# Optimization experiments

Hardware: AMD Instinct MI355X
Metric: run time of the kernel (lower is better)

## Reference

```python
import jax, jax.numpy as jnp
import numpy as np

EPS = 1e-8  # torch F.cosine_similarity default eps


def setup_inputs() -> dict:
    key = jax.random.key(0)
    k1, k2 = jax.random.split(key)
    xs_pad = jax.random.normal(k1, (8, 4096, 512), dtype=jnp.float32)
    spk_emb = jax.random.normal(k2, (8, 256, 512), dtype=jnp.float32)
    return {"xs_pad": xs_pad, "spk_emb": spk_emb}


def reference(xs_pad, spk_emb):
    # Faithful to F.cosine_similarity(x.unsqueeze(2), y.unsqueeze(1), dim=-1):
    #   dot(x, y) / (max(||x||, eps) * max(||y||, eps))
    # Implemented as L2-normalize then a batched GEMM -> (B, T, S), avoiding
    # the (B, T, S, D) broadcast intermediate.
    x_norm = jnp.maximum(jnp.linalg.norm(xs_pad, axis=-1, keepdims=True), EPS)
    y_norm = jnp.maximum(jnp.linalg.norm(spk_emb, axis=-1, keepdims=True), EPS)
    xn = xs_pad / x_norm          # (B, T, D)
    yn = spk_emb / y_norm         # (B, S, D)
    scores = jnp.einsum('btd,bsd->bts', xn, yn)  # (B, T, S)
    return scores
```

## Files before the change

### kernel.cpp

```cpp
#include <hip/hip_runtime.h>
#include <hip/hip_bf16.h>

#define BB 8
#define TT 4096
#define SS 256
#define DD 512
#define XROWS (BB * TT)
#define YROWS (BB * SS)

typedef __attribute__((ext_vector_type(8))) short short8;
typedef __attribute__((ext_vector_type(4))) float floatx4;

__device__ inline short f2bf(float f) {
  unsigned u = __builtin_bit_cast(unsigned, f);
  u += 0x7fffu + ((u >> 16) & 1u);
  return (short)(u >> 16);
}

__device__ inline short8 cvt8(float4 f0, float4 f1) {
  short8 o;
  o[0] = f2bf(f0.x);
  o[1] = f2bf(f0.y);
  o[2] = f2bf(f0.z);
  o[3] = f2bf(f0.w);
  o[4] = f2bf(f1.x);
  o[5] = f2bf(f1.y);
  o[6] = f2bf(f1.z);
  o[7] = f2bf(f1.w);
  return o;
}

__global__ __launch_bounds__(256) void cos_scale_kernel(
    const float* __restrict__ xs, const float* __restrict__ spk,
    float* __restrict__ xscale, float* __restrict__ yscale) {
  const int wave = threadIdx.x >> 6;
  const int lane = threadIdx.x & 63;
  int row = blockIdx.x * 4 + wave;
  const float* src;
  float* dst;
  if (row < XROWS) {
    src = xs + (size_t)row * DD;
    dst = xscale + row;
  } else {
    int r = row - XROWS;
    src = spk + (size_t)r * DD;
    dst = yscale + r;
  }
  const float4* s4 = (const float4*)src + lane * 2;
  float4 a = s4[0];
  float4 b = s4[1];
  float ss = a.x * a.x + a.y * a.y + a.z * a.z + a.w * a.w +
             b.x * b.x + b.y * b.y + b.z * b.z + b.w * b.w;
#pragma unroll
  for (int off = 32; off; off >>= 1) ss += __shfl_xor(ss, off, 64);
  if (lane == 0) *dst = 1.0f / fmaxf(sqrtf(ss), 1e-8f);
}

__global__ __launch_bounds__(256) void cos_gemm_kernel(
    const float* __restrict__ xs, const float* __restrict__ spk,
    const float* __restrict__ xscale, const float* __restrict__ yscale,
    float* __restrict__ out) {
  __shared__ float sA[128 * 64];
  __shared__ float sB[128 * 64];

  const int tid = threadIdx.x;
  const int wave = tid >> 6;
  const int lane = tid & 63;
  const int tn = blockIdx.x;
  const int tm = blockIdx.y;
  const int b = blockIdx.z;

  const float* Abase = xs + ((size_t)b * TT + tm * 128) * DD;
  const float* Bbase = spk + ((size_t)b * SS + tn * 128) * DD;

  floatx4 acc[4][4];
#pragma unroll
  for (int i = 0; i < 4; i++)
#pragma unroll
    for (int j = 0; j < 4; j++) acc[i][j] = (floatx4){0.f, 0.f, 0.f, 0.f};

  const int wm = wave >> 1;
  const int wn = wave & 1;
  const int quad = lane >> 4;
  const int l15 = lane & 15;

  int aoff[8];
#pragma unroll
  for (int j = 0; j < 8; j++) {
    int s = j * 256 + tid;
    int row = s >> 4;
    int blk = (s & 15) ^ (row & 15);
    aoff[j] = row * DD + blk * 4;
  }

  for (int kt = 0; kt < DD / 64; ++kt) {
#pragma unroll
    for (int j = 0; j < 8; j++) {
      const float* ga = Abase + aoff[j] + kt * 64;
      const float* gb = Bbase + aoff[j] + kt * 64;
      __builtin_amdgcn_global_load_lds(
          (const __attribute__((address_space(1))) unsigned int*)ga,
          (__attribute__((address_space(3))) unsigned int*)(sA +
              (j * 256 + wave * 64) * 4),
          16, 0, 0);
      __builtin_amdgcn_global_load_lds(
          (const __attribute__((address_space(1))) unsigned int*)gb,
          (__attribute__((address_space(3))) unsigned int*)(sB +
              (j * 256 + wave * 64) * 4),
          16, 0, 0);
    }
    __syncthreads();

#pragma unroll
    for (int ks = 0; ks < 2; ks++) {
      short8 af[4], bf[4];
      const int b0 = ks * 8 + quad * 2;
#pragma unroll
      for (int im = 0; im < 4; im++) {
        int row = wm * 64 + im * 16 + l15;
        int s0 = b0 ^ (row & 15);
        int s1 = (b0 + 1) ^ (row & 15);
        float4 f0 = *(const float4*)(sA + row * 64 + s0 * 4);
        float4 f1 = *(const float4*)(sA + row * 64 + s1 * 4);
        af[im] = cvt8(f0, f1);
      }
#pragma unroll
      for (int in = 0; in < 4; in++) {
        int row = wn * 64 + in * 16 + l15;
        int s0 = b0 ^ (row & 15);
        int s1 = (b0 + 1) ^ (row & 15);
        float4 f0 = *(const float4*)(sB + row * 64 + s0 * 4);
        float4 f1 = *(const float4*)(sB + row * 64 + s1 * 4);
        bf[in] = cvt8(f0, f1);
      }
#pragma unroll
      for (int im = 0; im < 4; im++)
#pragma unroll
        for (int in = 0; in < 4; in++)
          acc[im][in] = __builtin_amdgcn_mfma_f32_16x16x32_bf16(
              af[im], bf[in], acc[im][in], 0, 0, 0);
    }
    __syncthreads();
  }

  float* Obase = out + ((size_t)b * TT + tm * 128) * SS + tn * 128;
  const float* xsc = xscale + b * TT + tm * 128;
  const float* ysc = yscale + b * SS + tn * 128;
#pragma unroll
  for (int im = 0; im < 4; im++) {
#pragma unroll
    for (int in = 0; in < 4; in++) {
      int col = wn * 64 + in * 16 + l15;
      float yv = ysc[col];
#pragma unroll
      for (int r = 0; r < 4; r++) {
        int row = wm * 64 + im * 16 + quad * 4 + r;
        Obase[row * SS + col] = acc[im][in][r] * xsc[row] * yv;
      }
    }
  }
}

extern "C" void kernel_launch(void* const* d_in, const int* in_sizes, int n_in,
                              void* d_out, int out_size, void* d_ws,
                              size_t ws_size, hipStream_t stream) {
  const float* xs = (const float*)d_in[0];
  const float* spk = (const float*)d_in[1];
  float* out = (float*)d_out;

  float* xscale = (float*)d_ws;
  float* yscale = xscale + XROWS;

  hipLaunchKernelGGL(cos_scale_kernel, dim3((XROWS + YROWS) / 4), dim3(256), 0,
                     stream, xs, spk, xscale, yscale);
  hipLaunchKernelGGL(cos_gemm_kernel, dim3(SS / 128, TT / 128, BB), dim3(256),
                     0, stream, xs, spk, xscale, yscale, out);
}
```

Measured before the change: 124.9 us.

## Fuse row-norm computation into GEMM kernel using LDS-resident tiles

Removes the separate norm-scale kernel and computes the squared row norms of both operands inside the GEMM from the fp32 tiles already loaded into shared memory. Partial sums are reduced across lane quads with shuffles and stored as reciprocal scales in shared memory for the epilogue. This eliminates a full extra pass over the large input, a workspace round trip and one kernel launch. In exchange it adds extra FMA work per tile, more registers, and a redundant computation of the same norms by each tile sharing a row.

After: 123.8 us. About the same (-0.9%).

```diff
diff --git a/kernel.cpp b/kernel.cpp
--- a/kernel.cpp
+++ b/kernel.cpp
@@ -5,8 +5,6 @@
 #define TT 4096
 #define SS 256
 #define DD 512
-#define XROWS (BB * TT)
-#define YROWS (BB * SS)
 
 typedef __attribute__((ext_vector_type(8))) short short8;
 typedef __attribute__((ext_vector_type(4))) float floatx4;
@@ -30,38 +28,18 @@
   return o;
 }
 
-__global__ __launch_bounds__(256) void cos_scale_kernel(
-    const float* __restrict__ xs, const float* __restrict__ spk,
-    float* __restrict__ xscale, float* __restrict__ yscale) {
-  const int wave = threadIdx.x >> 6;
-  const int lane = threadIdx.x & 63;
-  int row = blockIdx.x * 4 + wave;
-  const float* src;
-  float* dst;
-  if (row < XROWS) {
-    src = xs + (size_t)row * DD;
-    dst = xscale + row;
-  } else {
-    int r = row - XROWS;
-    src = spk + (size_t)r * DD;
-    dst = yscale + r;
-  }
-  const float4* s4 = (const float4*)src + lane * 2;
-  float4 a = s4[0];
-  float4 b = s4[1];
-  float ss = a.x * a.x + a.y * a.y + a.z * a.z + a.w * a.w +
-             b.x * b.x + b.y * b.y + b.z * b.z + b.w * b.w;
-#pragma unroll
-  for (int off = 32; off; off >>= 1) ss += __shfl_xor(ss, off, 64);
-  if (lane == 0) *dst = 1.0f / fmaxf(sqrtf(ss), 1e-8f);
+__device__ inline float sq8(float4 f0, float4 f1) {
+  return f0.x * f0.x + f0.y * f0.y + f0.z * f0.z + f0.w * f0.w +
+         f1.x * f1.x + f1.y * f1.y + f1.z * f1.z + f1.w * f1.w;
 }
 
-__global__ __launch_bounds__(256) void cos_gemm_kernel(
+__global__ __launch_bounds__(256) void cos_fused_kernel(
     const float* __restrict__ xs, const float* __restrict__ spk,
-    const float* __restrict__ xscale, const float* __restrict__ yscale,
     float* __restrict__ out) {
   __shared__ float sA[128 * 64];
   __shared__ float sB[128 * 64];
+  __shared__ float scX[128];
+  __shared__ float scY[128];
 
   const int tid = threadIdx.x;
   const int wave = tid >> 6;
@@ -78,6 +56,9 @@
   for (int i = 0; i < 4; i++)
 #pragma unroll
     for (int j = 0; j < 4; j++) acc[i][j] = (floatx4){0.f, 0.f, 0.f, 0.f};
+
+  float sx[4] = {0.f, 0.f, 0.f, 0.f};
+  float sy[4] = {0.f, 0.f, 0.f, 0.f};
 
   const int wm = wave >> 1;
   const int wn = wave & 1;
@@ -122,6 +103,7 @@
         int s1 = (b0 + 1) ^ (row & 15);
         float4 f0 = *(const float4*)(sA + row * 64 + s0 * 4);
         float4 f1 = *(const float4*)(sA + row * 64 + s1 * 4);
+        sx[im] += sq8(f0, f1);
         af[im] = cvt8(f0, f1);
       }
 #pragma unroll
@@ -131,6 +113,7 @@
         int s1 = (b0 + 1) ^ (row & 15);
         float4 f0 = *(const float4*)(sB + row * 64 + s0 * 4);
         float4 f1 = *(const float4*)(sB + row * 64 + s1 * 4);
+        sy[in] += sq8(f0, f1);
         bf[in] = cvt8(f0, f1);
       }
 #pragma unroll
@@ -143,19 +126,33 @@
     __syncthreads();
   }
 
+#pragma unroll
+  for (int i = 0; i < 4; i++) {
+    sx[i] += __shfl_xor(sx[i], 16, 64);
+    sx[i] += __shfl_xor(sx[i], 32, 64);
+    sy[i] += __shfl_xor(sy[i], 16, 64);
+    sy[i] += __shfl_xor(sy[i], 32, 64);
+  }
+  if (quad == 0) {
+#pragma unroll
+    for (int i = 0; i < 4; i++) {
+      scX[wm * 64 + i * 16 + l15] = 1.0f / fmaxf(sqrtf(sx[i]), 1e-8f);
+      scY[wn * 64 + i * 16 + l15] = 1.0f / fmaxf(sqrtf(sy[i]), 1e-8f);
+    }
+  }
+  __syncthreads();
+
   float* Obase = out + ((size_t)b * TT + tm * 128) * SS + tn * 128;
-  const float* xsc = xscale + b * TT + tm * 128;
-  const float* ysc = yscale + b * SS + tn * 128;
 #pragma unroll
   for (int im = 0; im < 4; im++) {
 #pragma unroll
     for (int in = 0; in < 4; in++) {
       int col = wn * 64 + in * 16 + l15;
-      float yv = ysc[col];
+      float yv = scY[col];
 #pragma unroll
       for (int r = 0; r < 4; r++) {
         int row = wm * 64 + im * 16 + quad * 4 + r;
-        Obase[row * SS + col] = acc[im][in][r] * xsc[row] * yv;
+        Obase[row * SS + col] = acc[im][in][r] * scX[row] * yv;
       }
     }
   }
@@ -168,11 +165,6 @@
   const float* spk = (const float*)d_in[1];
   float* out = (float*)d_out;
 
-  float* xscale = (float*)d_ws;
-  float* yscale = xscale + XROWS;
-
-  hipLaunchKernelGGL(cos_scale_kernel, dim3((XROWS + YROWS) / 4), dim3(256), 0,
-                     stream, xs, spk, xscale, yscale);
-  hipLaunchKernelGGL(cos_gemm_kernel, dim3(SS / 128, TT / 128, BB), dim3(256),
-                     0, stream, xs, spk, xscale, yscale, out);
+  hipLaunchKernelGGL(cos_fused_kernel, dim3(SS / 128, TT / 128, BB), dim3(256),
+                     0, stream, xs, spk, out);
 }
```
